# Optimization experiments

Measured on AMD Instinct MI355X. Metric: run time of the kernel, lower is better.

## Reference

```python
import jax, jax.numpy as jnp
import numpy as np

N = 50000
E = 1600000
D_IN, D_H1, D_H2 = 256, 128, 64


def setup_inputs() -> dict:
    key = jax.random.key(0)
    ks = jax.random.split(key, 16)
    def lin(k, fan_in, fan_out):
        # torch nn.Linear default init: U(-1/sqrt(fan_in), 1/sqrt(fan_in))
        kw, kb = jax.random.split(k)
        bound = 1.0 / np.sqrt(fan_in)
        W = jax.random.uniform(kw, (fan_out, fan_in), jnp.float32, -bound, bound)
        b = jax.random.uniform(kb, (fan_out,), jnp.float32, -bound, bound)
        return W, b
    x = jax.random.normal(ks[0], (N, D_IN), jnp.float32)
    edge_index = jax.random.randint(ks[1], (2, E), 0, N, jnp.int64)
    edge_weight = jax.random.uniform(ks[2], (E,), jnp.float32)
    enc1_w, enc1_b = lin(ks[3], D_IN, D_H1)
    enc2_w, enc2_b = lin(ks[4], D_H1, D_H2)
    gcn1_w, gcn1_b = lin(ks[5], D_H2, D_H2)
    gcn2_w, gcn2_b = lin(ks[6], D_H2, D_H2)
    dec1_w, dec1_b = lin(ks[7], D_H2, D_H1)
    dec2_w, dec2_b = lin(ks[8], D_H1, D_IN)
    return dict(x=x, edge_index=edge_index, edge_weight=edge_weight,
                enc1_w=enc1_w, enc1_b=enc1_b, enc2_w=enc2_w, enc2_b=enc2_b,
                gcn1_w=gcn1_w, gcn1_b=gcn1_b, gcn2_w=gcn2_w, gcn2_b=gcn2_b,
                dec1_w=dec1_w, dec1_b=dec1_b, dec2_w=dec2_w, dec2_b=dec2_b)


def _gcn_conv(h, src, dst, w_all, W, b, n_nodes):
    # PyG GCNConv: h' = D^{-1/2}(A+I)D^{-1/2} (h W^T) + b; self-loops already in src/dst/w_all
    h = h @ W.T
    deg = jax.ops.segment_sum(w_all, dst, num_segments=n_nodes)
    dinv = jnp.where(deg > 0, jax.lax.rsqrt(jnp.maximum(deg, 1e-12)), 0.0)
    norm = dinv[src] * w_all * dinv[dst]                 # [E+N]
    msg = h[src] * norm[:, None]                         # gather + scale
    out = jax.ops.segment_sum(msg, dst, num_segments=n_nodes)  # scatter-add
    return out + b


def reference(x, edge_index, edge_weight,
              enc1_w, enc1_b, enc2_w, enc2_b,
              gcn1_w, gcn1_b, gcn2_w, gcn2_b,
              dec1_w, dec1_b, dec2_w, dec2_b):
    n = x.shape[0]
    # add self-loops (weight 1.0), as PyG GCNConv does by default
    loop = jnp.arange(n, dtype=edge_index.dtype)
    src = jnp.concatenate([edge_index[0], loop])
    dst = jnp.concatenate([edge_index[1], loop])
    w_all = jnp.concatenate([edge_weight, jnp.ones((n,), edge_weight.dtype)])

    h = jax.nn.relu(x @ enc1_w.T + enc1_b)
    h = jax.nn.relu(h @ enc2_w.T + enc2_b)
    h = jax.nn.relu(_gcn_conv(h, src, dst, w_all, gcn1_w, gcn1_b, n))
    h = jax.nn.relu(_gcn_conv(h, src, dst, w_all, gcn2_w, gcn2_b, n))
    h = jax.nn.relu(h @ dec1_w.T + dec1_b)
    h = h @ dec2_w.T + dec2_b
    return jax.nn.sigmoid(h)
```

## Files before the change

kernel.cpp:

```cpp
#include <hip/hip_runtime.h>


constexpr int NBLK = 128;
constexpr int GRP  = NBLK / 8;

typedef __attribute__((ext_vector_type(8))) short bf16x8;
typedef __attribute__((ext_vector_type(4))) float f32x4;

__device__ inline void split2(float f0, float f1, unsigned& hp, unsigned& lp) {
    unsigned u0 = __float_as_uint(f0), u1 = __float_as_uint(f1);
    hp = (u1 & 0xFFFF0000u) | (u0 >> 16);
    float r0 = f0 - __uint_as_float(u0 & 0xFFFF0000u);
    float r1 = f1 - __uint_as_float(u1 & 0xFFFF0000u);
    lp = (__float_as_uint(r1) & 0xFFFF0000u) | (__float_as_uint(r0) >> 16);
}

struct WSplitArgs {
    const float* src[6];
    unsigned short* hi[6];
    unsigned short* lo[6];
    int n[6];
};
__global__ __launch_bounds__(256) void split_w(WSplitArgs a) {
    const int L = blockIdx.y;
    const int i = blockIdx.x * 256 + threadIdx.x;
    if (i < a.n[L]) {
        float f = a.src[L][i];
        unsigned u = __float_as_uint(f);
        float r = f - __uint_as_float(u & 0xFFFF0000u);
        a.hi[L][i] = (unsigned short)(u >> 16);
        a.lo[L][i] = (unsigned short)(__float_as_uint(r) >> 16);
    }
}

template <int K, int M, int ACT, bool BIAS, int WM, int WN, int MF, int NF>
__global__ __launch_bounds__(256) void gemm_bd(const float* __restrict__ A,
                                               const unsigned short* __restrict__ Whp,
                                               const unsigned short* __restrict__ Wlp,
                                               const float* __restrict__ bias,
                                               float* __restrict__ C, int N) {
    static_assert(K % 64 == 0, "K%64");
    static_assert(WM * WN == 4, "4 waves");
    static_assert(WM * MF * 16 == 128, "BM=128");
    constexpr int KC = 64;
    constexpr int BN = WN * NF * 16;
    __shared__ unsigned Ah[128][36];
    __shared__ unsigned Al[128][36];

    const int tid      = threadIdx.x;
    const int nodeBase = blockIdx.x * 128;
    const int foff     = blockIdx.y * BN;

    const int srow = tid >> 4;
    const int sc4  = tid & 15;
    float4 av[8];

#pragma unroll
    for (int q = 0; q < 8; ++q) {
        const int gn = nodeBase + q * 16 + srow;
        av[q] = (gn < N) ? *(const float4*)(A + (size_t)gn * K + sc4 * 4)
                         : make_float4(0.f, 0.f, 0.f, 0.f);
    }

    f32x4 acc[MF][NF];
#pragma unroll
    for (int mf = 0; mf < MF; ++mf)
#pragma unroll
        for (int nf = 0; nf < NF; ++nf) acc[mf][nf] = (f32x4)0.f;

    const int lane = tid & 63;
    const int wid  = tid >> 6;
    const int wm   = wid / WN;
    const int wn   = wid % WN;
    const int fr   = lane & 15;
    const int fg   = lane >> 4;

    for (int kc = 0; kc < K; kc += KC) {
#pragma unroll
        for (int q = 0; q < 8; ++q) {
            unsigned h0, l0, h1, l1;
            split2(av[q].x, av[q].y, h0, l0);
            split2(av[q].z, av[q].w, h1, l1);
            const int r = q * 16 + srow;
            Ah[r][sc4 * 2] = h0; Ah[r][sc4 * 2 + 1] = h1;
            Al[r][sc4 * 2] = l0; Al[r][sc4 * 2 + 1] = l1;
        }
        __syncthreads();

        if (kc + KC < K) {
#pragma unroll
            for (int q = 0; q < 8; ++q) {
                const int gn = nodeBase + q * 16 + srow;
                av[q] = (gn < N)
                    ? *(const float4*)(A + (size_t)gn * K + kc + KC + sc4 * 4)
                    : make_float4(0.f, 0.f, 0.f, 0.f);
            }
        }

#pragma unroll
        for (int kf = 0; kf < 2; ++kf) {
            bf16x8 bh[NF], bl[NF];
#pragma unroll
            for (int nf = 0; nf < NF; ++nf) {
                const size_t wo = (size_t)(foff + wn * NF * 16 + nf * 16 + fr) * K
                                  + kc + kf * 32 + fg * 8;
                bh[nf] = *(const bf16x8*)(Whp + wo);
                bl[nf] = *(const bf16x8*)(Wlp + wo);
            }
            bf16x8 ah[MF], alo[MF];
#pragma unroll
            for (int mf = 0; mf < MF; ++mf) {
                const int r = wm * MF * 16 + mf * 16 + fr;
                ah[mf]  = *(const bf16x8*)&Ah[r][kf * 16 + fg * 4];
                alo[mf] = *(const bf16x8*)&Al[r][kf * 16 + fg * 4];
            }
#pragma unroll
            for (int mf = 0; mf < MF; ++mf)
#pragma unroll
                for (int nf = 0; nf < NF; ++nf) {
                    acc[mf][nf] = __builtin_amdgcn_mfma_f32_16x16x32_bf16(
                        ah[mf], bh[nf], acc[mf][nf], 0, 0, 0);
                    acc[mf][nf] = __builtin_amdgcn_mfma_f32_16x16x32_bf16(
                        alo[mf], bh[nf], acc[mf][nf], 0, 0, 0);
                    acc[mf][nf] = __builtin_amdgcn_mfma_f32_16x16x32_bf16(
                        ah[mf], bl[nf], acc[mf][nf], 0, 0, 0);
                }
        }
        __syncthreads();
    }

#pragma unroll
    for (int nf = 0; nf < NF; ++nf) {
        const int feat = foff + wn * NF * 16 + nf * 16 + fr;
        const float bv = BIAS ? bias[feat] : 0.f;
#pragma unroll
        for (int mf = 0; mf < MF; ++mf) {
            const int node0 = nodeBase + wm * MF * 16 + mf * 16 + fg * 4;
#pragma unroll
            for (int i = 0; i < 4; ++i) {
                const int node = node0 + i;
                if (node < N) {
                    float x = acc[mf][nf][i] + bv;
                    if constexpr (ACT == 1) x = fmaxf(x, 0.f);
                    if constexpr (ACT == 2) x = 1.f / (1.f + __expf(-x));
                    C[(size_t)node * M + feat] = x;
                }
            }
        }
    }
}


__global__ __launch_bounds__(256) void count_k(const int* __restrict__ ei,
                                               int* __restrict__ cnt,
                                               int NB, int E) {
    __shared__ int hist[784];
    const int tid = threadIdx.x;
    for (int i = tid; i < NB; i += 256) hist[i] = 0;
    __syncthreads();
    const int chunk = (E + NBLK - 1) / NBLK;
    const int lo = blockIdx.x * chunk;
    const int hi = min(lo + chunk, E);
    for (int e = lo + tid; e < hi; e += 256) {
        int d = ei[E + e];
        atomicAdd(&hist[d >> 6], 1);
    }
    __syncthreads();
    const int r = blockIdx.x & 7, g = blockIdx.x >> 3;
    for (int i = tid; i < NB; i += 256)
        cnt[i * NBLK + r * GRP + g] = hist[i];
}

__global__ __launch_bounds__(256) void scan1(const int* __restrict__ cnt,
                                             int* __restrict__ pos,
                                             int* __restrict__ bs, int n) {
    __shared__ int s[256];
    const int t = threadIdx.x;
    const int i0 = blockIdx.x * 512 + 2 * t;
    int c0 = (i0     < n) ? cnt[i0]     : 0;
    int c1 = (i0 + 1 < n) ? cnt[i0 + 1] : 0;
    int c = c0 + c1;
    s[t] = c;
    __syncthreads();
    for (int off = 1; off < 256; off <<= 1) {
        int v = (t >= off) ? s[t - off] : 0;
        __syncthreads();
        s[t] += v;
        __syncthreads();
    }
    int excl = s[t] - c;
    if (i0     < n) pos[i0]     = excl;
    if (i0 + 1 < n) pos[i0 + 1] = excl + c0;
    if (t == 255) bs[blockIdx.x] = s[255];
}

__global__ __launch_bounds__(256) void scan_tops(int* __restrict__ bs, int nb) {
    __shared__ int s[256];
    int t = threadIdx.x;
    int v = (t < nb) ? bs[t] : 0;
    s[t] = v;
    __syncthreads();
    for (int off = 1; off < 256; off <<= 1) {
        int u = (t >= off) ? s[t - off] : 0;
        __syncthreads();
        s[t] += u;
        __syncthreads();
    }
    if (t < nb) bs[t] = s[t] - v;
}

__global__ __launch_bounds__(256) void scan2(int* __restrict__ pos,
                                             const int* __restrict__ bs,
                                             int* __restrict__ bucketBase,
                                             int n, int NB, int E) {
    const int t = threadIdx.x;
    const int i0 = blockIdx.x * 512 + 2 * t;
    const int add = bs[blockIdx.x];
#pragma unroll
    for (int c = 0; c < 2; ++c) {
        int i = i0 + c;
        if (i < n) {
            int v = pos[i] + add;
            pos[i] = v;
            if ((i & (NBLK - 1)) == 0) bucketBase[i >> 7] = v;
        }
    }
    if (blockIdx.x == 0 && t == 0) bucketBase[NB] = E;
}

__global__ __launch_bounds__(256) void place_k(const int* __restrict__ ei,
                                               const float* __restrict__ w,
                                               const int* __restrict__ pos,
                                               int2* __restrict__ ebuf,
                                               int NB, int E) {
    __shared__ int cur[784];
    const int tid = threadIdx.x;
    const int r = blockIdx.x & 7, g = blockIdx.x >> 3;
    for (int i = tid; i < NB; i += 256) cur[i] = pos[i * NBLK + r * GRP + g];
    __syncthreads();
    const int chunk = (E + NBLK - 1) / NBLK;
    const int lo = blockIdx.x * chunk;
    const int hi = min(lo + chunk, E);
    for (int e = lo + tid; e < hi; e += 256) {
        int s = ei[e];
        int d = ei[E + e];
        float wv = w[e];
        int p = atomicAdd(&cur[d >> 6], 1);
        ebuf[p] = make_int2(s | ((d & 63) << 26), __float_as_int(wv));
    }
}

__global__ __launch_bounds__(256) void bucket_build(const int2* __restrict__ ebuf,
                                                    const int* __restrict__ bucketBase,
                                                    int2* __restrict__ sn,
                                                    int* __restrict__ row,
                                                    float* __restrict__ dinv,
                                                    int N, int E) {
    __shared__ int   lh[64];
    __shared__ float ldg[64];
    __shared__ int   sc[64];
    __shared__ int   lofs[64];
    const int tid  = threadIdx.x;
    const int base = bucketBase[blockIdx.x];
    const int end  = bucketBase[blockIdx.x + 1];

    if (tid < 64) { lh[tid] = 0; ldg[tid] = 0.f; }
    __syncthreads();
    for (int i = base + tid; i < end; i += 256) {
        int2 v = ebuf[i];
        int dl = ((unsigned)v.x) >> 26;
        atomicAdd(&lh[dl], 1);
        atomicAdd(&ldg[dl], __int_as_float(v.y));
    }
    __syncthreads();
    if (tid < 64) sc[tid] = lh[tid];
    __syncthreads();
    for (int off = 1; off < 64; off <<= 1) {
        int v = (tid < 64 && tid >= off) ? sc[tid - off] : 0;
        __syncthreads();
        if (tid < 64) sc[tid] += v;
        __syncthreads();
    }
    if (tid < 64) {
        int excl = sc[tid] - lh[tid];
        int d = (blockIdx.x << 6) + tid;
        if (d < N) {
            row[d]  = base + excl;
            dinv[d] = rsqrtf(fmaxf(1.0f + ldg[tid], 1e-12f));
        }
        lofs[tid] = base + excl;
    }
    __syncthreads();
    for (int i = base + tid; i < end; i += 256) {
        int2 v = ebuf[i];
        unsigned u = (unsigned)v.x;
        int dl = u >> 26;
        int s  = u & 0x03FFFFFF;
        int p  = atomicAdd(&lofs[dl], 1);
        sn[p] = make_int2(s, v.y);
    }
    if (blockIdx.x == 0 && tid == 0) row[N] = E;
}

__global__ __launch_bounds__(256) void scale_pay(int2* __restrict__ sn,
                                                 const float* __restrict__ dinv,
                                                 int E) {
    int p = blockIdx.x * 256 + threadIdx.x;
    if (p < E) {
        int2 v = sn[p];
        sn[p] = make_int2(v.x, __float_as_int(__int_as_float(v.y) * dinv[v.x]));
    }
}

__global__ __launch_bounds__(256) void gcn_agg(const float* __restrict__ t,
                                               const int2* __restrict__ sn,
                                               const int* __restrict__ row,
                                               const float* __restrict__ dinv,
                                               const float* __restrict__ bias,
                                               float* __restrict__ out, int N) {
    const int lane = threadIdx.x & 63;
    int i = __builtin_amdgcn_readfirstlane((int)(blockIdx.x * 4) + (threadIdx.x >> 6));
    if (i >= N) return;
    float di   = dinv[i];
    float self = t[(size_t)i * 64 + lane];
    float acc  = 0.f;
    int p  = row[i];
    int pe = row[i + 1];
    for (; p + 4 <= pe; p += 4) {
        int2 v0 = sn[p];
        int2 v1 = sn[p + 1];
        int2 v2 = sn[p + 2];
        int2 v3 = sn[p + 3];
        acc += t[(size_t)v0.x * 64 + lane] * __int_as_float(v0.y);
        acc += t[(size_t)v1.x * 64 + lane] * __int_as_float(v1.y);
        acc += t[(size_t)v2.x * 64 + lane] * __int_as_float(v2.y);
        acc += t[(size_t)v3.x * 64 + lane] * __int_as_float(v3.y);
    }
    for (; p < pe; ++p) {
        int2 v = sn[p];
        acc += t[(size_t)v.x * 64 + lane] * __int_as_float(v.y);
    }
    float x = (acc + self * di) * di + bias[lane];
    out[(size_t)i * 64 + lane] = fmaxf(x, 0.f);
}

extern "C" void kernel_launch(void* const* d_in, const int* in_sizes, int n_in,
                              void* d_out, int out_size, void* d_ws, size_t ws_size,
                              hipStream_t stream) {
    const float* x      = (const float*)d_in[0];
    const int*   ei     = (const int*)d_in[1];
    const float* ew     = (const float*)d_in[2];
    const float* enc1_w = (const float*)d_in[3];
    const float* enc1_b = (const float*)d_in[4];
    const float* enc2_w = (const float*)d_in[5];
    const float* enc2_b = (const float*)d_in[6];
    const float* gcn1_w = (const float*)d_in[7];
    const float* gcn1_b = (const float*)d_in[8];
    const float* gcn2_w = (const float*)d_in[9];
    const float* gcn2_b = (const float*)d_in[10];
    const float* dec1_w = (const float*)d_in[11];
    const float* dec1_b = (const float*)d_in[12];
    const float* dec2_w = (const float*)d_in[13];
    const float* dec2_b = (const float*)d_in[14];

    const int N  = in_sizes[0] / 256;
    const int E  = in_sizes[2];
    const int NB = (N + 63) / 64;
    const int NCNT = NB * NBLK;
    const int NS   = (NCNT + 511) / 512;

    float* ws   = (float*)d_ws;
    float* bufA = ws;
    int2*  sn   = (int2*)bufA;
    float* bufC = bufA + (size_t)2 * E;
    int2*  ebuf = (int2*)bufC;
    float* bufB = bufA + (size_t)N * 128;
    float* dinv = bufB + (size_t)N * 64;
    int*   row  = (int*)(dinv + N);
    int*   cnt  = row + (N + 1);
    int*   pos  = cnt + NCNT;
    int*   bucketBase = pos + NCNT;
    int*   bs   = bucketBase + (NB + 1);
    unsigned short* whi = (unsigned short*)(bs + 256);
    unsigned short* wlo = whi + 90112;

    const int gemmGrid = (N + 127) / 128;
    const int nBlkE    = (E + 255) / 256;

    WSplitArgs wa;
    const float* wsrc[6] = {enc1_w, enc2_w, gcn1_w, gcn2_w, dec1_w, dec2_w};
    const int    wsz[6]  = {32768, 8192, 4096, 4096, 8192, 32768};
    const int    woff[6] = {0, 32768, 40960, 45056, 49152, 57344};
    for (int l = 0; l < 6; ++l) {
        wa.src[l] = wsrc[l];
        wa.hi[l]  = whi + woff[l];
        wa.lo[l]  = wlo + woff[l];
        wa.n[l]   = wsz[l];
    }
    split_w<<<dim3(128, 6), 256, 0, stream>>>(wa);

    gemm_bd<256, 128, 1, true, 2, 2, 4, 4><<<dim3(gemmGrid, 1), 256, 0, stream>>>(
        x, whi + woff[0], wlo + woff[0], enc1_b, bufA, N);
    gemm_bd<128, 64, 1, true, 4, 1, 2, 4><<<dim3(gemmGrid, 1), 256, 0, stream>>>(
        bufA, whi + woff[1], wlo + woff[1], enc2_b, bufB, N);

    count_k<<<NBLK, 256, 0, stream>>>(ei, cnt, NB, E);
    scan1<<<NS, 256, 0, stream>>>(cnt, pos, bs, NCNT);
    scan_tops<<<1, 256, 0, stream>>>(bs, NS);
    scan2<<<NS, 256, 0, stream>>>(pos, bs, bucketBase, NCNT, NB, E);
    place_k<<<NBLK, 256, 0, stream>>>(ei, ew, pos, ebuf, NB, E);
    bucket_build<<<NB, 256, 0, stream>>>(ebuf, bucketBase, sn, row, dinv, N, E);
    scale_pay<<<nBlkE, 256, 0, stream>>>(sn, dinv, E);

    gemm_bd<64, 64, 0, false, 4, 1, 2, 4><<<dim3(gemmGrid, 1), 256, 0, stream>>>(
        bufB, whi + woff[2], wlo + woff[2], nullptr, bufC, N);
    gcn_agg<<<(N + 3) / 4, 256, 0, stream>>>(bufC, sn, row, dinv, gcn1_b, bufB, N);

    gemm_bd<64, 64, 0, false, 4, 1, 2, 4><<<dim3(gemmGrid, 1), 256, 0, stream>>>(
        bufB, whi + woff[3], wlo + woff[3], nullptr, bufC, N);
    gcn_agg<<<(N + 3) / 4, 256, 0, stream>>>(bufC, sn, row, dinv, gcn2_b, bufB, N);

    gemm_bd<64, 128, 1, true, 2, 2, 4, 4><<<dim3(gemmGrid, 1), 256, 0, stream>>>(
        bufB, whi + woff[4], wlo + woff[4], dec1_b, bufA, N);
    gemm_bd<128, 256, 2, true, 2, 2, 4, 4><<<dim3(gemmGrid, 2), 256, 0, stream>>>(
        bufA, whi + woff[5], wlo + woff[5], dec2_b, (float*)d_out, N);
}
```

Before: 468.7 us.

## Store activations as pre-split bf16 hi/lo pairs and drop LDS staging in GEMMs

The shared-memory GEMM, which split fp32 activations into bf16 hi/lo halves inside every kernel, is replaced by a register-only kernel that reads MFMA fragments straight from global memory. Producer kernels (the GEMM epilogues and gcn_agg) now write activations already split into hi/lo bf16 arrays, so the consumer GEMMs skip the split and the LDS round trip with its barriers. Tiles shrink to 64x64 with 128-thread blocks, which gives more blocks in the grid. The workspace layout is reorganised to hold the split buffers. The risk is uncoalesced direct global fragment loads and the loss of the reuse that shared memory provided across waves.

Measured after the change: 493.2 us. 5.2% more time.

```diff
diff --git a/kernel.cpp b/kernel.cpp
--- a/kernel.cpp
+++ b/kernel.cpp
@@ -13,6 +13,16 @@
     float r0 = f0 - __uint_as_float(u0 & 0xFFFF0000u);
     float r1 = f1 - __uint_as_float(u1 & 0xFFFF0000u);
     lp = (__float_as_uint(r1) & 0xFFFF0000u) | (__float_as_uint(r0) >> 16);
+}
+
+struct Bf16Pair { bf16x8 h, l; };
+__device__ inline Bf16Pair split8(float4 a, float4 b) {
+    union { unsigned u[4]; bf16x8 v; } H, L;
+    split2(a.x, a.y, H.u[0], L.u[0]);
+    split2(a.z, a.w, H.u[1], L.u[1]);
+    split2(b.x, b.y, H.u[2], L.u[2]);
+    split2(b.z, b.w, H.u[3], L.u[3]);
+    Bf16Pair p; p.h = H.v; p.l = L.v; return p;
 }
 
 struct WSplitArgs {
@@ -33,109 +43,86 @@
     }
 }
 
-template <int K, int M, int ACT, bool BIAS, int WM, int WN, int MF, int NF>
-__global__ __launch_bounds__(256) void gemm_bd(const float* __restrict__ A,
-                                               const unsigned short* __restrict__ Whp,
-                                               const unsigned short* __restrict__ Wlp,
-                                               const float* __restrict__ bias,
-                                               float* __restrict__ C, int N) {
-    static_assert(K % 64 == 0, "K%64");
-    static_assert(WM * WN == 4, "4 waves");
-    static_assert(WM * MF * 16 == 128, "BM=128");
-    constexpr int KC = 64;
-    constexpr int BN = WN * NF * 16;
-    __shared__ unsigned Ah[128][36];
-    __shared__ unsigned Al[128][36];
-
-    const int tid      = threadIdx.x;
-    const int nodeBase = blockIdx.x * 128;
-    const int foff     = blockIdx.y * BN;
-
-    const int srow = tid >> 4;
-    const int sc4  = tid & 15;
-    float4 av[8];
-
-#pragma unroll
-    for (int q = 0; q < 8; ++q) {
-        const int gn = nodeBase + q * 16 + srow;
-        av[q] = (gn < N) ? *(const float4*)(A + (size_t)gn * K + sc4 * 4)
-                         : make_float4(0.f, 0.f, 0.f, 0.f);
-    }
-
-    f32x4 acc[MF][NF];
-#pragma unroll
-    for (int mf = 0; mf < MF; ++mf)
-#pragma unroll
-        for (int nf = 0; nf < NF; ++nf) acc[mf][nf] = (f32x4)0.f;
-
+template <int K, int M, int ACT, bool BIAS, bool AF32, int OUT>
+__global__ __launch_bounds__(128) void gemm_pp(
+        const unsigned short* __restrict__ Ahp,
+        const unsigned short* __restrict__ Alp,
+        const float* __restrict__ Af,
+        const unsigned short* __restrict__ Whp,
+        const unsigned short* __restrict__ Wlp,
+        const float* __restrict__ bias,
+        float* __restrict__ Cf,
+        unsigned short* __restrict__ Chi,
+        unsigned short* __restrict__ Clo, int N) {
+    static_assert(K % 32 == 0, "K%32");
+    constexpr int MF = 2;
+    constexpr int NF = 4;
+
+    const int tid  = threadIdx.x;
     const int lane = tid & 63;
     const int wid  = tid >> 6;
-    const int wm   = wid / WN;
-    const int wn   = wid % WN;
     const int fr   = lane & 15;
     const int fg   = lane >> 4;
-
-    for (int kc = 0; kc < K; kc += KC) {
-#pragma unroll
-        for (int q = 0; q < 8; ++q) {
-            unsigned h0, l0, h1, l1;
-            split2(av[q].x, av[q].y, h0, l0);
-            split2(av[q].z, av[q].w, h1, l1);
-            const int r = q * 16 + srow;
-            Ah[r][sc4 * 2] = h0; Ah[r][sc4 * 2 + 1] = h1;
-            Al[r][sc4 * 2] = l0; Al[r][sc4 * 2 + 1] = l1;
-        }
-        __syncthreads();
-
-        if (kc + KC < K) {
-#pragma unroll
-            for (int q = 0; q < 8; ++q) {
-                const int gn = nodeBase + q * 16 + srow;
-                av[q] = (gn < N)
-                    ? *(const float4*)(A + (size_t)gn * K + kc + KC + sc4 * 4)
-                    : make_float4(0.f, 0.f, 0.f, 0.f);
+    const int rowBase = blockIdx.x * 64 + wid * 32;
+    const int foff    = blockIdx.y * 64;
+
+    f32x4 acc[MF][NF];
+#pragma unroll
+    for (int mf = 0; mf < MF; ++mf)
+#pragma unroll
+        for (int nf = 0; nf < NF; ++nf) acc[mf][nf] = (f32x4)0.f;
+
+    int arow[MF];
+#pragma unroll
+    for (int mf = 0; mf < MF; ++mf) {
+        int r = rowBase + mf * 16 + fr;
+        arow[mf] = (r < N) ? r : (N - 1);
+    }
+
+#pragma unroll 2
+    for (int kf = 0; kf < K / 32; ++kf) {
+        const int ko = kf * 32 + fg * 8;
+        bf16x8 ah[MF], al[MF], bh[NF], bl[NF];
+#pragma unroll
+        for (int mf = 0; mf < MF; ++mf) {
+            if constexpr (AF32) {
+                const float* ap = Af + (size_t)arow[mf] * K + ko;
+                float4 f0 = *(const float4*)(ap);
+                float4 f1 = *(const float4*)(ap + 4);
+                Bf16Pair p = split8(f0, f1);
+                ah[mf] = p.h; al[mf] = p.l;
+            } else {
+                const size_t ao = (size_t)arow[mf] * K + ko;
+                ah[mf] = *(const bf16x8*)(Ahp + ao);
+                al[mf] = *(const bf16x8*)(Alp + ao);
             }
         }
-
-#pragma unroll
-        for (int kf = 0; kf < 2; ++kf) {
-            bf16x8 bh[NF], bl[NF];
+#pragma unroll
+        for (int nf = 0; nf < NF; ++nf) {
+            const size_t wo = (size_t)(foff + nf * 16 + fr) * K + ko;
+            bh[nf] = *(const bf16x8*)(Whp + wo);
+            bl[nf] = *(const bf16x8*)(Wlp + wo);
+        }
+#pragma unroll
+        for (int mf = 0; mf < MF; ++mf)
 #pragma unroll
             for (int nf = 0; nf < NF; ++nf) {
-                const size_t wo = (size_t)(foff + wn * NF * 16 + nf * 16 + fr) * K
-                                  + kc + kf * 32 + fg * 8;
-                bh[nf] = *(const bf16x8*)(Whp + wo);
-                bl[nf] = *(const bf16x8*)(Wlp + wo);
+                acc[mf][nf] = __builtin_amdgcn_mfma_f32_16x16x32_bf16(
+                    ah[mf], bh[nf], acc[mf][nf], 0, 0, 0);
+                acc[mf][nf] = __builtin_amdgcn_mfma_f32_16x16x32_bf16(
+                    al[mf], bh[nf], acc[mf][nf], 0, 0, 0);
+                acc[mf][nf] = __builtin_amdgcn_mfma_f32_16x16x32_bf16(
+                    ah[mf], bl[nf], acc[mf][nf], 0, 0, 0);
             }
-            bf16x8 ah[MF], alo[MF];
-#pragma unroll
-            for (int mf = 0; mf < MF; ++mf) {
-                const int r = wm * MF * 16 + mf * 16 + fr;
-                ah[mf]  = *(const bf16x8*)&Ah[r][kf * 16 + fg * 4];
-                alo[mf] = *(const bf16x8*)&Al[r][kf * 16 + fg * 4];
-            }
-#pragma unroll
-            for (int mf = 0; mf < MF; ++mf)
-#pragma unroll
-                for (int nf = 0; nf < NF; ++nf) {
-                    acc[mf][nf] = __builtin_amdgcn_mfma_f32_16x16x32_bf16(
-                        ah[mf], bh[nf], acc[mf][nf], 0, 0, 0);
-                    acc[mf][nf] = __builtin_amdgcn_mfma_f32_16x16x32_bf16(
-                        alo[mf], bh[nf], acc[mf][nf], 0, 0, 0);
-                    acc[mf][nf] = __builtin_amdgcn_mfma_f32_16x16x32_bf16(
-                        ah[mf], bl[nf], acc[mf][nf], 0, 0, 0);
-                }
-        }
-        __syncthreads();
     }
 
 #pragma unroll
     for (int nf = 0; nf < NF; ++nf) {
-        const int feat = foff + wn * NF * 16 + nf * 16 + fr;
+        const int feat = foff + nf * 16 + fr;
         const float bv = BIAS ? bias[feat] : 0.f;
 #pragma unroll
         for (int mf = 0; mf < MF; ++mf) {
-            const int node0 = nodeBase + wm * MF * 16 + mf * 16 + fg * 4;
+            const int node0 = rowBase + mf * 16 + fg * 4;
 #pragma unroll
             for (int i = 0; i < 4; ++i) {
                 const int node = node0 + i;
@@ -143,7 +130,15 @@
                     float x = acc[mf][nf][i] + bv;
                     if constexpr (ACT == 1) x = fmaxf(x, 0.f);
                     if constexpr (ACT == 2) x = 1.f / (1.f + __expf(-x));
-                    C[(size_t)node * M + feat] = x;
+                    const size_t idx = (size_t)node * M + feat;
+                    if constexpr (OUT == 0) {
+                        Cf[idx] = x;
+                    } else {
+                        unsigned u = __float_as_uint(x);
+                        Chi[idx] = (unsigned short)(u >> 16);
+                        float r = x - __uint_as_float(u & 0xFFFF0000u);
+                        Clo[idx] = (unsigned short)(__float_as_uint(r) >> 16);
+                    }
                 }
             }
         }
@@ -317,7 +312,9 @@
                                                const int* __restrict__ row,
                                                const float* __restrict__ dinv,
                                                const float* __restrict__ bias,
-                                               float* __restrict__ out, int N) {
+                                               unsigned short* __restrict__ outh,
+                                               unsigned short* __restrict__ outl,
+                                               int N) {
     const int lane = threadIdx.x & 63;
     int i = __builtin_amdgcn_readfirstlane((int)(blockIdx.x * 4) + (threadIdx.x >> 6));
     if (i >= N) return;
@@ -340,8 +337,12 @@
         int2 v = sn[p];
         acc += t[(size_t)v.x * 64 + lane] * __int_as_float(v.y);
     }
-    float x = (acc + self * di) * di + bias[lane];
-    out[(size_t)i * 64 + lane] = fmaxf(x, 0.f);
+    float x = fmaxf((acc + self * di) * di + bias[lane], 0.f);
+    const size_t idx = (size_t)i * 64 + lane;
+    unsigned u = __float_as_uint(x);
+    outh[idx] = (unsigned short)(u >> 16);
+    float r = x - __uint_as_float(u & 0xFFFF0000u);
+    outl[idx] = (unsigned short)(__float_as_uint(r) >> 16);
 }
 
 extern "C" void kernel_launch(void* const* d_in, const int* in_sizes, int n_in,
@@ -369,22 +370,27 @@
     const int NCNT = NB * NBLK;
     const int NS   = (NCNT + 511) / 512;
 
-    float* ws   = (float*)d_ws;
-    float* bufA = ws;
-    int2*  sn   = (int2*)bufA;
-    float* bufC = bufA + (size_t)2 * E;
-    int2*  ebuf = (int2*)bufC;
-    float* bufB = bufA + (size_t)N * 128;
-    float* dinv = bufB + (size_t)N * 64;
+    float* bufT = (float*)d_ws;
+    unsigned short* R2 = (unsigned short*)(bufT + (size_t)N * 64);
+    unsigned short* h1h = R2;
+    unsigned short* h1l = R2 + (size_t)N * 128;
+    int2* sn   = (int2*)R2;
+    int2* ebuf = sn + E;
+    unsigned short* h5h = R2;
+    unsigned short* h5l = R2 + (size_t)N * 128;
+    unsigned short* R3 = R2 + (size_t)2 * N * 128;
+    unsigned short* gh = R3;
+    unsigned short* gl = R3 + (size_t)N * 64;
+    unsigned short* whi = R3 + (size_t)2 * N * 64;
+    unsigned short* wlo = whi + 90112;
+    float* dinv = (float*)(wlo + 90112);
     int*   row  = (int*)(dinv + N);
     int*   cnt  = row + (N + 1);
     int*   pos  = cnt + NCNT;
     int*   bucketBase = pos + NCNT;
     int*   bs   = bucketBase + (NB + 1);
-    unsigned short* whi = (unsigned short*)(bs + 256);
-    unsigned short* wlo = whi + 90112;
-
-    const int gemmGrid = (N + 127) / 128;
+
+    const int gemmGrid = (N + 63) / 64;
     const int nBlkE    = (E + 255) / 256;
 
     WSplitArgs wa;
@@ -399,10 +405,12 @@
     }
     split_w<<<dim3(128, 6), 256, 0, stream>>>(wa);
 
-    gemm_bd<256, 128, 1, true, 2, 2, 4, 4><<<dim3(gemmGrid, 1), 256, 0, stream>>>(
-        x, whi + woff[0], wlo + woff[0], enc1_b, bufA, N);
-    gemm_bd<128, 64, 1, true, 4, 1, 2, 4><<<dim3(gemmGrid, 1), 256, 0, stream>>>(
-        bufA, whi + woff[1], wlo + woff[1], enc2_b, bufB, N);
+    gemm_pp<256, 128, 1, true, true, 1><<<dim3(gemmGrid, 2), 128, 0, stream>>>(
+        nullptr, nullptr, x, whi + woff[0], wlo + woff[0], enc1_b,
+        nullptr, h1h, h1l, N);
+    gemm_pp<128, 64, 1, true, false, 1><<<dim3(gemmGrid, 1), 128, 0, stream>>>(
+        h1h, h1l, nullptr, whi + woff[1], wlo + woff[1], enc2_b,
+        nullptr, gh, gl, N);
 
     count_k<<<NBLK, 256, 0, stream>>>(ei, cnt, NB, E);
     scan1<<<NS, 256, 0, stream>>>(cnt, pos, bs, NCNT);
@@ -412,16 +420,20 @@
     bucket_build<<<NB, 256, 0, stream>>>(ebuf, bucketBase, sn, row, dinv, N, E);
     scale_pay<<<nBlkE, 256, 0, stream>>>(sn, dinv, E);
 
-    gemm_bd<64, 64, 0, false, 4, 1, 2, 4><<<dim3(gemmGrid, 1), 256, 0, stream>>>(
-        bufB, whi + woff[2], wlo + woff[2], nullptr, bufC, N);
-    gcn_agg<<<(N + 3) / 4, 256, 0, stream>>>(bufC, sn, row, dinv, gcn1_b, bufB, N);
-
-    gemm_bd<64, 64, 0, false, 4, 1, 2, 4><<<dim3(gemmGrid, 1), 256, 0, stream>>>(
-        bufB, whi + woff[3], wlo + woff[3], nullptr, bufC, N);
-    gcn_agg<<<(N + 3) / 4, 256, 0, stream>>>(bufC, sn, row, dinv, gcn2_b, bufB, N);
-
-    gemm_bd<64, 128, 1, true, 2, 2, 4, 4><<<dim3(gemmGrid, 1), 256, 0, stream>>>(
-        bufB, whi + woff[4], wlo + woff[4], dec1_b, bufA, N);
-    gemm_bd<128, 256, 2, true, 2, 2, 4, 4><<<dim3(gemmGrid, 2), 256, 0, stream>>>(
-        bufA, whi + woff[5], wlo + woff[5], dec2_b, (float*)d_out, N);
-}
+    gemm_pp<64, 64, 0, false, false, 0><<<dim3(gemmGrid, 1), 128, 0, stream>>>(
+        gh, gl, nullptr, whi + woff[2], wlo + woff[2], nullptr,
+        bufT, nullptr, nullptr, N);
+    gcn_agg<<<(N + 3) / 4, 256, 0, stream>>>(bufT, sn, row, dinv, gcn1_b, gh, gl, N);
+
+    gemm_pp<64, 64, 0, false, false, 0><<<dim3(gemmGrid, 1), 128, 0, stream>>>(
+        gh, gl, nullptr, whi + woff[3], wlo + woff[3], nullptr,
+        bufT, nullptr, nullptr, N);
+    gcn_agg<<<(N + 3) / 4, 256, 0, stream>>>(bufT, sn, row, dinv, gcn2_b, gh, gl, N);
+
+    gemm_pp<64, 128, 1, true, false, 1><<<dim3(gemmGrid, 2), 128, 0, stream>>>(
+        gh, gl, nullptr, whi + woff[4], wlo + woff[4], dec1_b,
+        nullptr, h5h, h5l, N);
+    gemm_pp<128, 256, 2, true, false, 0><<<dim3(gemmGrid, 4), 128, 0, stream>>>(
+        h5h, h5l, nullptr, whi + woff[5], wlo + woff[5], dec2_b,
+        (float*)d_out, nullptr, nullptr, N);
+}
```

## Shrink GEMM tiles to 64x64 with XCD-aware block remapping and vectorized LDS stores

Applied to the files above, without the earlier changes.

Replaces the 128-row GEMM tile with a fixed 64x64 tile using 4 waves in a 2x2 layout. The grid is now split over output features, and block IDs are remapped so that consecutive tiles land on the same XCD. The A tile is split into bf16 hi/lo halves and written to LDS as 16-byte vectors. The aim is more blocks for occupancy and better L2 locality across XCDs, at the cost of lower per-block reuse and reloading A once for each feature tile.

New measurement: 458.9 us. 1.02x faster.

```diff
diff --git a/kernel.cpp b/kernel.cpp
--- a/kernel.cpp
+++ b/kernel.cpp
@@ -13,6 +13,16 @@
     float r0 = f0 - __uint_as_float(u0 & 0xFFFF0000u);
     float r1 = f1 - __uint_as_float(u1 & 0xFFFF0000u);
     lp = (__float_as_uint(r1) & 0xFFFF0000u) | (__float_as_uint(r0) >> 16);
+}
+
+struct Bf16Pair { bf16x8 h, l; };
+__device__ inline Bf16Pair split8(float4 a, float4 b) {
+    union { unsigned u[4]; bf16x8 v; } H, L;
+    split2(a.x, a.y, H.u[0], L.u[0]);
+    split2(a.z, a.w, H.u[1], L.u[1]);
+    split2(b.x, b.y, H.u[2], L.u[2]);
+    split2(b.z, b.w, H.u[3], L.u[3]);
+    Bf16Pair p; p.h = H.v; p.l = L.v; return p;
 }
 
 struct WSplitArgs {
@@ -33,95 +43,95 @@
     }
 }
 
-template <int K, int M, int ACT, bool BIAS, int WM, int WN, int MF, int NF>
-__global__ __launch_bounds__(256) void gemm_bd(const float* __restrict__ A,
+template <int K, int M, int ACT, bool BIAS>
+__global__ __launch_bounds__(256) void gemm_sp(const float* __restrict__ A,
                                                const unsigned short* __restrict__ Whp,
                                                const unsigned short* __restrict__ Wlp,
                                                const float* __restrict__ bias,
                                                float* __restrict__ C, int N) {
     static_assert(K % 64 == 0, "K%64");
-    static_assert(WM * WN == 4, "4 waves");
-    static_assert(WM * MF * 16 == 128, "BM=128");
-    constexpr int KC = 64;
-    constexpr int BN = WN * NF * 16;
-    __shared__ unsigned Ah[128][36];
-    __shared__ unsigned Al[128][36];
-
-    const int tid      = threadIdx.x;
-    const int nodeBase = blockIdx.x * 128;
-    const int foff     = blockIdx.y * BN;
-
-    const int srow = tid >> 4;
-    const int sc4  = tid & 15;
-    float4 av[8];
-
-#pragma unroll
-    for (int q = 0; q < 8; ++q) {
-        const int gn = nodeBase + q * 16 + srow;
-        av[q] = (gn < N) ? *(const float4*)(A + (size_t)gn * K + sc4 * 4)
-                         : make_float4(0.f, 0.f, 0.f, 0.f);
-    }
-
-    f32x4 acc[MF][NF];
-#pragma unroll
-    for (int mf = 0; mf < MF; ++mf)
-#pragma unroll
-        for (int nf = 0; nf < NF; ++nf) acc[mf][nf] = (f32x4)0.f;
-
+    constexpr int KS = 64;
+    __shared__ __align__(16) unsigned short Ah[64][72];
+    __shared__ __align__(16) unsigned short Al[64][72];
+
+    const int gx  = gridDim.x;
+    const int nwg = gx * gridDim.y;
+    {
+    }
+    const int o    = blockIdx.y * gx + blockIdx.x;
+    const int xcd  = o & 7;
+    const int idx  = o >> 3;
+    const int q    = nwg >> 3, rr = nwg & 7;
+    const int wgid = (xcd < rr ? xcd * (q + 1) : rr * (q + 1) + (xcd - rr) * q) + idx;
+    const int foff     = (wgid % gx) * 64;
+    const int nodeBase = (wgid / gx) * 64;
+
+    const int tid  = threadIdx.x;
     const int lane = tid & 63;
     const int wid  = tid >> 6;
-    const int wm   = wid / WN;
-    const int wn   = wid % WN;
+    const int wm   = wid >> 1;
+    const int wn   = wid & 1;
     const int fr   = lane & 15;
     const int fg   = lane >> 4;
 
-    for (int kc = 0; kc < K; kc += KC) {
-#pragma unroll
-        for (int q = 0; q < 8; ++q) {
-            unsigned h0, l0, h1, l1;
-            split2(av[q].x, av[q].y, h0, l0);
-            split2(av[q].z, av[q].w, h1, l1);
-            const int r = q * 16 + srow;
-            Ah[r][sc4 * 2] = h0; Ah[r][sc4 * 2 + 1] = h1;
-            Al[r][sc4 * 2] = l0; Al[r][sc4 * 2 + 1] = l1;
-        }
-        __syncthreads();
-
-        if (kc + KC < K) {
-#pragma unroll
-            for (int q = 0; q < 8; ++q) {
-                const int gn = nodeBase + q * 16 + srow;
-                av[q] = (gn < N)
-                    ? *(const float4*)(A + (size_t)gn * K + kc + KC + sc4 * 4)
-                    : make_float4(0.f, 0.f, 0.f, 0.f);
+    const int srow = tid >> 2;
+    const int sc0  = (tid & 3) * 16;
+    int grow = nodeBase + srow;
+    if (grow >= N) grow = N - 1;
+    const float* aptr = A + (size_t)grow * K + sc0;
+
+    float4 av[4];
+#pragma unroll
+    for (int i = 0; i < 4; ++i) av[i] = *(const float4*)(aptr + i * 4);
+
+    f32x4 acc[2][2];
+#pragma unroll
+    for (int mf = 0; mf < 2; ++mf)
+#pragma unroll
+        for (int nf = 0; nf < 2; ++nf) acc[mf][nf] = (f32x4)0.f;
+
+    for (int kc = 0; kc < K; kc += KS) {
+        {
+            Bf16Pair p0 = split8(av[0], av[1]);
+            Bf16Pair p1 = split8(av[2], av[3]);
+            *(bf16x8*)&Ah[srow][sc0]     = p0.h;
+            *(bf16x8*)&Ah[srow][sc0 + 8] = p1.h;
+            *(bf16x8*)&Al[srow][sc0]     = p0.l;
+            *(bf16x8*)&Al[srow][sc0 + 8] = p1.l;
+        }
+        __syncthreads();
+
+        if (kc + KS < K) {
+#pragma unroll
+            for (int i = 0; i < 4; ++i)
+                av[i] = *(const float4*)(aptr + kc + KS + i * 4);
+        }
+
+#pragma unroll
+        for (int kf = 0; kf < 2; ++kf) {
+            const int kcol = kf * 32 + fg * 8;
+            bf16x8 ah[2], al[2], bh[2], bl[2];
+#pragma unroll
+            for (int mf = 0; mf < 2; ++mf) {
+                const int r = wm * 32 + mf * 16 + fr;
+                ah[mf] = *(const bf16x8*)&Ah[r][kcol];
+                al[mf] = *(const bf16x8*)&Al[r][kcol];
             }
-        }
-
-#pragma unroll
-        for (int kf = 0; kf < 2; ++kf) {
-            bf16x8 bh[NF], bl[NF];
-#pragma unroll
-            for (int nf = 0; nf < NF; ++nf) {
-                const size_t wo = (size_t)(foff + wn * NF * 16 + nf * 16 + fr) * K
-                                  + kc + kf * 32 + fg * 8;
+#pragma unroll
+            for (int nf = 0; nf < 2; ++nf) {
+                const size_t wo = (size_t)(foff + wn * 32 + nf * 16 + fr) * K
+                                  + kc + kcol;
                 bh[nf] = *(const bf16x8*)(Whp + wo);
                 bl[nf] = *(const bf16x8*)(Wlp + wo);
             }
-            bf16x8 ah[MF], alo[MF];
-#pragma unroll
-            for (int mf = 0; mf < MF; ++mf) {
-                const int r = wm * MF * 16 + mf * 16 + fr;
-                ah[mf]  = *(const bf16x8*)&Ah[r][kf * 16 + fg * 4];
-                alo[mf] = *(const bf16x8*)&Al[r][kf * 16 + fg * 4];
-            }
-#pragma unroll
-            for (int mf = 0; mf < MF; ++mf)
-#pragma unroll
-                for (int nf = 0; nf < NF; ++nf) {
+#pragma unroll
+            for (int mf = 0; mf < 2; ++mf)
+#pragma unroll
+                for (int nf = 0; nf < 2; ++nf) {
                     acc[mf][nf] = __builtin_amdgcn_mfma_f32_16x16x32_bf16(
                         ah[mf], bh[nf], acc[mf][nf], 0, 0, 0);
                     acc[mf][nf] = __builtin_amdgcn_mfma_f32_16x16x32_bf16(
-                        alo[mf], bh[nf], acc[mf][nf], 0, 0, 0);
+                        al[mf], bh[nf], acc[mf][nf], 0, 0, 0);
                     acc[mf][nf] = __builtin_amdgcn_mfma_f32_16x16x32_bf16(
                         ah[mf], bl[nf], acc[mf][nf], 0, 0, 0);
                 }
@@ -130,12 +140,12 @@
     }
 
 #pragma unroll
-    for (int nf = 0; nf < NF; ++nf) {
-        const int feat = foff + wn * NF * 16 + nf * 16 + fr;
+    for (int nf = 0; nf < 2; ++nf) {
+        const int feat = foff + wn * 32 + nf * 16 + fr;
         const float bv = BIAS ? bias[feat] : 0.f;
 #pragma unroll
-        for (int mf = 0; mf < MF; ++mf) {
-            const int node0 = nodeBase + wm * MF * 16 + mf * 16 + fg * 4;
+        for (int mf = 0; mf < 2; ++mf) {
+            const int node0 = nodeBase + wm * 32 + mf * 16 + fg * 4;
 #pragma unroll
             for (int i = 0; i < 4; ++i) {
                 const int node = node0 + i;
@@ -384,8 +394,8 @@
     unsigned short* whi = (unsigned short*)(bs + 256);
     unsigned short* wlo = whi + 90112;
 
-    const int gemmGrid = (N + 127) / 128;
-    const int nBlkE    = (E + 255) / 256;
+    const int nodeTiles = (N + 63) / 64;
+    const int nBlkE     = (E + 255) / 256;
 
     WSplitArgs wa;
     const float* wsrc[6] = {enc1_w, enc2_w, gcn1_w, gcn2_w, dec1_w, dec2_w};
@@ -399,9 +409,9 @@
     }
     split_w<<<dim3(128, 6), 256, 0, stream>>>(wa);
 
-    gemm_bd<256, 128, 1, true, 2, 2, 4, 4><<<dim3(gemmGrid, 1), 256, 0, stream>>>(
+    gemm_sp<256, 128, 1, true><<<dim3(2, nodeTiles), 256, 0, stream>>>(
         x, whi + woff[0], wlo + woff[0], enc1_b, bufA, N);
-    gemm_bd<128, 64, 1, true, 4, 1, 2, 4><<<dim3(gemmGrid, 1), 256, 0, stream>>>(
+    gemm_sp<128, 64, 1, true><<<dim3(1, nodeTiles), 256, 0, stream>>>(
         bufA, whi + woff[1], wlo + woff[1], enc2_b, bufB, N);
 
     count_k<<<NBLK, 256, 0, stream>>>(ei, cnt, NB, E);
@@ -412,16 +422,16 @@
     bucket_build<<<NB, 256, 0, stream>>>(ebuf, bucketBase, sn, row, dinv, N, E);
     scale_pay<<<nBlkE, 256, 0, stream>>>(sn, dinv, E);
 
-    gemm_bd<64, 64, 0, false, 4, 1, 2, 4><<<dim3(gemmGrid, 1), 256, 0, stream>>>(
+    gemm_sp<64, 64, 0, false><<<dim3(1, nodeTiles), 256, 0, stream>>>(
         bufB, whi + woff[2], wlo + woff[2], nullptr, bufC, N);
     gcn_agg<<<(N + 3) / 4, 256, 0, stream>>>(bufC, sn, row, dinv, gcn1_b, bufB, N);
 
-    gemm_bd<64, 64, 0, false, 4, 1, 2, 4><<<dim3(gemmGrid, 1), 256, 0, stream>>>(
+    gemm_sp<64, 64, 0, false><<<dim3(1, nodeTiles), 256, 0, stream>>>(
         bufB, whi + woff[3], wlo + woff[3], nullptr, bufC, N);
     gcn_agg<<<(N + 3) / 4, 256, 0, stream>>>(bufC, sn, row, dinv, gcn2_b, bufB, N);
 
-    gemm_bd<64, 128, 1, true, 2, 2, 4, 4><<<dim3(gemmGrid, 1), 256, 0, stream>>>(
+    gemm_sp<64, 128, 1, true><<<dim3(2, nodeTiles), 256, 0, stream>>>(
         bufB, whi + woff[4], wlo + woff[4], dec1_b, bufA, N);
-    gemm_bd<128, 256, 2, true, 2, 2, 4, 4><<<dim3(gemmGrid, 2), 256, 0, stream>>>(
+    gemm_sp<128, 256, 2, true><<<dim3(4, nodeTiles), 256, 0, stream>>>(
         bufA, whi + woff[5], wlo + woff[5], dec2_b, (float*)d_out, N);
 }
```
